# Optimization experiments

Measured on AMD Instinct MI355X. Metric: run time of the kernel, lower is better.

The kernel has to match this reference:

```python
import jax, jax.numpy as jnp
import numpy as np
from jax import lax

B, H, W = 2, 1024, 1024
STRIDE = 32
HF, WF = H // STRIDE, W // STRIDE
C_FM = 2048
A = 9                                       # anchors per location
PRE = 2000                                  # pre-NMS top-k
TOPN = 1000                                 # post-NMS proposals per image
POOL = 7
FC = 256
NUM_CLS = 21
NMS_TH = 0.7


def make_anchors():
    scales = jnp.array([128., 256., 512.])
    ratios = jnp.array([0.5, 1., 2.])
    ws = (scales[:, None] / jnp.sqrt(ratios)[None, :]).reshape(-1)   # [9]
    hs = (scales[:, None] * jnp.sqrt(ratios)[None, :]).reshape(-1)   # [9]
    cx = (jnp.arange(WF) + 0.5) * STRIDE
    cy = (jnp.arange(HF) + 0.5) * STRIDE
    cyg, cxg = jnp.meshgrid(cy, cx, indexing='ij')                   # [HF,WF]
    cxg, cyg = cxg[..., None], cyg[..., None]                        # [HF,WF,1]
    x1 = cxg - ws / 2; y1 = cyg - hs / 2
    x2 = cxg + ws / 2; y2 = cyg + hs / 2
    return jnp.stack([x1, y1, x2, y2], -1).reshape(-1, 4)            # [HF*WF*9,4]


def decode(boxes, deltas):
    w = boxes[..., 2] - boxes[..., 0]
    h = boxes[..., 3] - boxes[..., 1]
    cx = boxes[..., 0] + 0.5 * w
    cy = boxes[..., 1] + 0.5 * h
    dx, dy = deltas[..., 0], deltas[..., 1]
    dw = jnp.clip(deltas[..., 2], -4.0, 4.0)
    dh = jnp.clip(deltas[..., 3], -4.0, 4.0)
    ncx = cx + dx * w; ncy = cy + dy * h
    nw = w * jnp.exp(dw); nh = h * jnp.exp(dh)
    return jnp.stack([ncx - 0.5 * nw, ncy - 0.5 * nh,
                      ncx + 0.5 * nw, ncy + 0.5 * nh], -1)


def clip_boxes(boxes):
    lim = jnp.array([W - 1., H - 1., W - 1., H - 1.])
    return jnp.clip(boxes, 0.0, lim)


def iou_mat(a, b):
    area_a = (a[:, 2] - a[:, 0]) * (a[:, 3] - a[:, 1])
    area_b = (b[:, 2] - b[:, 0]) * (b[:, 3] - b[:, 1])
    lt = jnp.maximum(a[:, None, :2], b[None, :, :2])
    rb = jnp.minimum(a[:, None, 2:], b[None, :, 2:])
    wh = jnp.clip(rb - lt, 0.0)
    inter = wh[..., 0] * wh[..., 1]
    return inter / (area_a[:, None] + area_b[None, :] - inter + 1e-9)


def nms_one(boxes, scores):
    s, idx = lax.top_k(scores, PRE)          # pre-NMS top-k, score-sorted
    b = boxes[idx]                           # [PRE,4]
    iou = iou_mat(b, b)                      # [PRE,PRE]
    ar = jnp.arange(PRE)

    def body(i, keep):
        sup = (iou[i] > NMS_TH) & keep[i] & (ar > i)
        return keep & (~sup)

    keep = lax.fori_loop(0, PRE, body, jnp.ones(PRE, bool))
    ms = jnp.where(keep, s, -1e30)
    s2, j = lax.top_k(ms, TOPN)
    valid = s2 > -1e29
    sel = b[j] * valid[:, None].astype(b.dtype)
    return sel, valid


def roi_align_one(fm, roi):
    # fm: [C,HF,WF], roi: [4] in image coords -> [C,POOL,POOL]
    scale = 1.0 / STRIDE
    x1, y1, x2, y2 = roi[0] * scale, roi[1] * scale, roi[2] * scale, roi[3] * scale
    xs = jnp.clip(x1 + (jnp.arange(POOL) + 0.5) * (x2 - x1) / POOL, 0.0, WF - 1.0)
    ys = jnp.clip(y1 + (jnp.arange(POOL) + 0.5) * (y2 - y1) / POOL, 0.0, HF - 1.0)
    x0 = jnp.floor(xs); y0 = jnp.floor(ys)
    wx = xs - x0; wy = ys - y0
    x0i = x0.astype(jnp.int32); x1i = jnp.minimum(x0i + 1, WF - 1)
    y0i = y0.astype(jnp.int32); y1i = jnp.minimum(y0i + 1, HF - 1)
    gy0 = fm[:, y0i, :]; gy1 = fm[:, y1i, :]          # [C,7,WF]
    f00 = gy0[:, :, x0i]; f01 = gy0[:, :, x1i]        # [C,7,7]
    f10 = gy1[:, :, x0i]; f11 = gy1[:, :, x1i]
    wy_ = wy[None, :, None]; wx_ = wx[None, None, :]
    return (f00 * (1 - wy_) * (1 - wx_) + f01 * (1 - wy_) * wx_
            + f10 * wy_ * (1 - wx_) + f11 * wy_ * wx_)


def conv(x, w, b, stride, padding):
    y = lax.conv_general_dilated(x, w, (stride, stride), padding,
                                 dimension_numbers=('NCHW', 'OIHW', 'NCHW'))
    return y + b[None, :, None, None]


def setup_inputs() -> dict:
    key = jax.random.key(0)
    ks = jax.random.split(key, 12)
    f32 = jnp.float32
    inp = {
        'x': jax.random.normal(ks[0], (B, 3, H, W), f32),
        'backbone_w': jax.random.normal(ks[1], (C_FM, 3, STRIDE, STRIDE), f32) * 0.02,
        'backbone_b': jnp.zeros((C_FM,), f32),
        'rpn_w': jax.random.normal(ks[2], (512, C_FM, 3, 3), f32) * 0.01,
        'rpn_b': jnp.zeros((512,), f32),
        'rpn_cls_w': jax.random.normal(ks[3], (2 * A, 512, 1, 1), f32) * 0.02,
        'rpn_cls_b': jnp.zeros((2 * A,), f32),
        'rpn_reg_w': jax.random.normal(ks[4], (4 * A, 512, 1, 1), f32) * 0.02,
        'rpn_reg_b': jnp.zeros((4 * A,), f32),
        'fc1_w': jax.random.normal(ks[5], (C_FM * POOL * POOL, FC), f32) * 0.005,
        'fc1_b': jnp.zeros((FC,), f32),
        'fc2_w': jax.random.normal(ks[6], (FC, FC), f32) * 0.05,
        'fc2_b': jnp.zeros((FC,), f32),
        'cls_w': jax.random.normal(ks[7], (FC, NUM_CLS), f32) * 0.05,
        'cls_b': jnp.zeros((NUM_CLS,), f32),
        'reg_w': jax.random.normal(ks[8], (FC, 4), f32) * 0.05,
        'reg_b': jnp.zeros((4,), f32),
    }
    return inp


def reference(x, backbone_w, backbone_b, rpn_w, rpn_b, rpn_cls_w, rpn_cls_b,
              rpn_reg_w, rpn_reg_b, fc1_w, fc1_b, fc2_w, fc2_b,
              cls_w, cls_b, reg_w, reg_b):
    # backbone (stride-32 patch conv stand-in for resnet50-small)
    fm = jax.nn.relu(conv(x, backbone_w, backbone_b, STRIDE, 'VALID'))   # [B,2048,32,32]

    anchors = make_anchors()                                             # [N,4], N=HF*WF*9
    anchors = jnp.broadcast_to(anchors, (B,) + anchors.shape)

    # RPN head
    h = jax.nn.relu(conv(fm, rpn_w, rpn_b, 1, 'SAME'))                   # [B,512,32,32]
    cls = conv(h, rpn_cls_w, rpn_cls_b, 1, 'SAME')                       # [B,18,32,32]
    reg = conv(h, rpn_reg_w, rpn_reg_b, 1, 'SAME')                       # [B,36,32,32]
    cls = cls.transpose(0, 2, 3, 1).reshape(B, -1, 2)
    reg = reg.transpose(0, 2, 3, 1).reshape(B, -1, 4)
    fg = jax.nn.softmax(cls, axis=-1)[..., 1]                            # [B,N]

    # proposals: decode -> clip -> NMS filter
    proposals = clip_boxes(decode(anchors, reg))                         # [B,N,4]
    props, valid = jax.vmap(nms_one)(proposals, fg)                      # [B,1000,4], [B,1000]

    # ROI pooling (bilinear, 1 sample/bin, spatial_scale=1/32)
    roi = jax.vmap(jax.vmap(roi_align_one, (None, 0)), (0, 0))(fm, props)  # [B,1000,C,7,7]
    vm = valid.astype(fm.dtype)[..., None]
    roi = roi.reshape(B, TOPN, -1) * vm                                  # [B,1000,100352]

    # detection head
    h1 = jax.nn.relu(jnp.einsum('bnf,fk->bnk', roi, fc1_w) + fc1_b)
    h2 = jax.nn.relu(jnp.einsum('bnk,kj->bnj', h1, fc2_w) + fc2_b)
    cls_scores = (jnp.einsum('bnj,jc->bnc', h2, cls_w) + cls_b) * vm
    reg_preds = (jnp.einsum('bnj,jr->bnr', h2, reg_w) + reg_b) * vm

    detections = clip_boxes(decode(props, reg_preds)) * vm
    return detections, cls_scores
```

## Files before the change

### kernel.cpp

```cpp
#include <hip/hip_runtime.h>

#define PRE 2000
#define TOPN 1000

typedef __attribute__((ext_vector_type(8))) short short8t;
typedef __attribute__((ext_vector_type(4))) float f32x4;
typedef unsigned short ushort_t;

__device__ inline unsigned short bf16_rne(float x) {
    unsigned u = __float_as_uint(x);
    unsigned r = u + 0x7FFFu + ((u >> 16) & 1u);
    return (unsigned short)(r >> 16);
}

__device__ inline void split3_bf16(float x, unsigned short& h, unsigned short& m,
                                   unsigned short& l) {
    h = bf16_rne(x);
    float hf = __uint_as_float((unsigned)h << 16);
    float r1 = x - hf;
    m = bf16_rne(r1);
    float mf = __uint_as_float((unsigned)m << 16);
    l = bf16_rne(r1 - mf);
}


__global__ __launch_bounds__(256, 4) void k_fused(
    const ushort_t* __restrict__ Aq, const ushort_t* __restrict__ Bq,
    ushort_t* __restrict__ T,
    const unsigned* __restrict__ mask, unsigned* __restrict__ keep)
{
    if (blockIdx.x < 2) {
        if (threadIdx.x >= 64) return;
        const int b = blockIdx.x;
        const int lane = threadIdx.x;
        unsigned kw = (lane < 62) ? 0xFFFFFFFFu : (lane == 62 ? 0xFFFFu : 0u);
        const unsigned* mbase = mask + (size_t)b * PRE * 63;
        bool ld = (lane < 63);

        unsigned buf[16];
#pragma unroll
        for (int d = 0; d < 16; d++)
            buf[d] = ld ? mbase[(size_t)d * 63 + lane] : 0u;

        for (int g = 0; g < PRE; g += 16) {
#pragma unroll
            for (int d = 0; d < 16; d++) {
                int i = g + d;
                unsigned row = buf[d];
                int ip = i + 16;
                buf[d] = (ld && ip < PRE) ? mbase[(size_t)ip * 63 + lane] : 0u;
                unsigned wv = (unsigned)__shfl((int)kw, i >> 5);
                if ((wv >> (i & 31)) & 1u)
                    kw &= ~row;
            }
        }
        if (lane < 63) keep[b * 63 + lane] = kw;
        return;
    }

    const int flat = blockIdx.x - 2;
    const int xcd  = flat & 7;
    const int jj   = flat >> 3;
    const int wg   = xcd * 196 + jj;
    const int b    = wg / 784;
    const int rem  = wg - b * 784;
    const int nt   = rem >> 3;
    const int mt   = rem & 7;

    const int tid  = threadIdx.x;
    const int wid  = tid >> 6, lane = tid & 63;
    const int wm_g = (wid >> 1) * 4;
    const int wn_g = (wid & 1) * 4;

    f32x4 acc[4][4];
#pragma unroll
    for (int i = 0; i < 4; i++)
#pragma unroll
        for (int j = 0; j < 4; j++) acc[i][j] = (f32x4){0.f, 0.f, 0.f, 0.f};

    const size_t aoff = (size_t)b * 2097152 + (size_t)mt * 262144
                      + (size_t)wm_g * 512 + (size_t)lane * 8;
    const size_t boff = (size_t)nt * 262144 + (size_t)wn_g * 512 + (size_t)lane * 8;
    const ushort_t* pA = Aq + aoff;
    const ushort_t* pB = Bq + boff;

    for (int ks = 0; ks < 64; ks++) {
        const size_t so = (size_t)ks * 4096;
        short8t a[4], bb[4];
#pragma unroll
        for (int f = 0; f < 4; f++) {
            a[f]  = *(const short8t*)(pA + so + f * 512);
            bb[f] = *(const short8t*)(pB + so + f * 512);
        }
#pragma unroll
        for (int mf = 0; mf < 4; mf++)
#pragma unroll
            for (int nf = 0; nf < 4; nf++)
                acc[mf][nf] = __builtin_amdgcn_mfma_f32_16x16x32_bf16(
                    a[mf], bb[nf], acc[mf][nf], 0, 0, 0);
    }

    ushort_t* Tb = T + (size_t)b * 12845056;
    const int rbase = (lane >> 4) * 4;
    const int lrow  = lane & 15;
#pragma unroll
    for (int mf = 0; mf < 4; mf++) {
#pragma unroll
        for (int nf = 0; nf < 4; nf++) {
            int col = nt * 128 + (wn_g + nf) * 16 + lrow;
#pragma unroll
            for (int r = 0; r < 4; r++) {
                int row = mt * 128 + (wm_g + mf) * 16 + rbase + r;
                Tb[(size_t)row * 12544 + col] = bf16_rne(acc[mf][nf][r]);
            }
        }
    }
}


__global__ __launch_bounds__(256, 2) void k_gemm6(
    const ushort_t* __restrict__ A0, const ushort_t* __restrict__ A1,
    const ushort_t* __restrict__ A2,
    const ushort_t* __restrict__ B0, const ushort_t* __restrict__ B1,
    const ushort_t* __restrict__ B2,
    float* __restrict__ C, int ks_per_z, int KS_TOT, int ldc)
{
    const int tid  = threadIdx.x;
    const int wid  = tid >> 6, lane = tid & 63;
    const int wm_g = (wid >> 1) * 4;
    const int wn_g = (wid & 1) * 4;
    const int mt   = blockIdx.x;
    const int nt   = blockIdx.y;
    const int z    = blockIdx.z;

    f32x4 acc[4][4];
#pragma unroll
    for (int i = 0; i < 4; i++)
#pragma unroll
        for (int j = 0; j < 4; j++) acc[i][j] = (f32x4){0.f, 0.f, 0.f, 0.f};

    const size_t aoff = (size_t)mt * KS_TOT * 4096 + (size_t)wm_g * 512 + (size_t)lane * 8;
    const size_t boff = (size_t)nt * KS_TOT * 4096 + (size_t)wn_g * 512 + (size_t)lane * 8;
    const ushort_t* pA0 = A0 + aoff;
    const ushort_t* pA1 = A1 + aoff;
    const ushort_t* pA2 = A2 + aoff;
    const ushort_t* pB0 = B0 + boff;
    const ushort_t* pB1 = B1 + boff;
    const ushort_t* pB2 = B2 + boff;

    const int ks0 = z * ks_per_z;
    for (int ks = ks0; ks < ks0 + ks_per_z; ks++) {
        const size_t so = (size_t)ks * 4096;
        short8t a0[4], a1[4], a2[4], b0[4], b1[4], b2[4];
#pragma unroll
        for (int f = 0; f < 4; f++) {
            a0[f] = *(const short8t*)(pA0 + so + f * 512);
            a1[f] = *(const short8t*)(pA1 + so + f * 512);
            a2[f] = *(const short8t*)(pA2 + so + f * 512);
            b0[f] = *(const short8t*)(pB0 + so + f * 512);
            b1[f] = *(const short8t*)(pB1 + so + f * 512);
            b2[f] = *(const short8t*)(pB2 + so + f * 512);
        }
#pragma unroll
        for (int mf = 0; mf < 4; mf++)
#pragma unroll
            for (int nf = 0; nf < 4; nf++) {
                f32x4 c = acc[mf][nf];
                c = __builtin_amdgcn_mfma_f32_16x16x32_bf16(a0[mf], b0[nf], c, 0, 0, 0);
                c = __builtin_amdgcn_mfma_f32_16x16x32_bf16(a0[mf], b1[nf], c, 0, 0, 0);
                c = __builtin_amdgcn_mfma_f32_16x16x32_bf16(a1[mf], b0[nf], c, 0, 0, 0);
                c = __builtin_amdgcn_mfma_f32_16x16x32_bf16(a0[mf], b2[nf], c, 0, 0, 0);
                c = __builtin_amdgcn_mfma_f32_16x16x32_bf16(a2[mf], b0[nf], c, 0, 0, 0);
                c = __builtin_amdgcn_mfma_f32_16x16x32_bf16(a1[mf], b1[nf], c, 0, 0, 0);
                acc[mf][nf] = c;
            }
    }

    float* Cz = C + (size_t)z * (gridDim.x * 128) * ldc;
    const int rbase = (lane >> 4) * 4;
    const int lrow  = lane & 15;
#pragma unroll
    for (int mf = 0; mf < 4; mf++) {
#pragma unroll
        for (int nf = 0; nf < 4; nf++) {
            int col = nt * 128 + (wn_g + nf) * 16 + lrow;
#pragma unroll
            for (int r = 0; r < 4; r++) {
                int row = mt * 128 + (wm_g + mf) * 16 + rbase + r;
                Cz[(size_t)row * ldc + col] = acc[mf][nf][r];
            }
        }
    }
}


__global__ void k_convW3(const float* __restrict__ src,
                         ushort_t* __restrict__ D0, ushort_t* __restrict__ D1,
                         ushort_t* __restrict__ D2,
                         int K_LD, int k_base, int KS_TOT)
{
    int t = blockIdx.x * 256 + threadIdx.x;
    int per = KS_TOT << 9;
    int mt = t / per, rem = t - mt * per;
    int ks = rem >> 9, g = (rem >> 6) & 7, l = rem & 63;
    int m  = mt * 128 + g * 16 + (l & 15);
    int k0 = k_base + ks * 32 + ((l >> 4) << 3);
    const float* sp = src + (size_t)m * K_LD + k0;
    short8t v0, v1, v2;
#pragma unroll
    for (int j = 0; j < 8; j++) {
        unsigned short h, mm_, lo;
        split3_bf16(sp[j], h, mm_, lo);
        v0[j] = (short)h; v1[j] = (short)mm_; v2[j] = (short)lo;
    }
    *(short8t*)&D0[(size_t)t * 8] = v0;
    *(short8t*)&D1[(size_t)t * 8] = v1;
    *(short8t*)&D2[(size_t)t * 8] = v2;
}

__global__ void k_convX3(const float* __restrict__ X,
                         ushort_t* __restrict__ D0, ushort_t* __restrict__ D1,
                         ushort_t* __restrict__ D2)
{
    int t = blockIdx.x * 256 + threadIdx.x;
    if (t >= 786432) return;
    int per = 96 << 9;
    int nt = t / per, rem = t - nt * per;
    int ks = rem >> 9, g = (rem >> 6) & 7, l = rem & 63;
    int n  = nt * 128 + g * 16 + (l & 15);
    int bimg = n >> 10, pn = n & 1023;
    int oy = pn >> 5, ox = pn & 31;
    int k0 = ks * 32 + ((l >> 4) << 3);
    int ic = k0 >> 10, kr = k0 & 1023;
    int ky = kr >> 5, kx0 = kr & 31;
    const float* sp = X + (((size_t)(bimg * 3 + ic) * 1024) + oy * 32 + ky) * 1024
                        + ox * 32 + kx0;
    short8t v0, v1, v2;
#pragma unroll
    for (int j = 0; j < 8; j++) {
        unsigned short h, mm_, lo;
        split3_bf16(sp[j], h, mm_, lo);
        v0[j] = (short)h; v1[j] = (short)mm_; v2[j] = (short)lo;
    }
    *(short8t*)&D0[(size_t)t * 8] = v0;
    *(short8t*)&D1[(size_t)t * 8] = v1;
    *(short8t*)&D2[(size_t)t * 8] = v2;
}

__global__ void k_convR3(const float* __restrict__ fm,
                         ushort_t* __restrict__ D0, ushort_t* __restrict__ D1,
                         ushort_t* __restrict__ D2, int k_base, int KS_TOT)
{
    int t = blockIdx.x * 256 + threadIdx.x;
    int per = KS_TOT << 9;
    if (t >= 16 * per) return;
    int nt = t / per, rem = t - nt * per;
    int ks = rem >> 9, g = (rem >> 6) & 7, l = rem & 63;
    int n  = nt * 128 + g * 16 + (l & 15);
    int bimg = n >> 10, pn = n & 1023;
    int y = pn >> 5, x = pn & 31;
    int kg = k_base + ks * 32 + ((l >> 4) << 3);
    int ic = kg / 9;
    int r9 = kg - ic * 9;
    int ky = r9 / 3;
    int kx = r9 - ky * 3;
    short8t v0, v1, v2;
#pragma unroll
    for (int j = 0; j < 8; j++) {
        int yy = y + ky - 1, xx = x + kx - 1;
        float v = 0.f;
        if (yy >= 0 && yy < 32 && xx >= 0 && xx < 32)
            v = fm[(((size_t)(bimg * 2048 + ic)) * 32 + yy) * 32 + xx];
        unsigned short h, mm_, lo;
        split3_bf16(v, h, mm_, lo);
        v0[j] = (short)h; v1[j] = (short)mm_; v2[j] = (short)lo;
        kx++;
        if (kx == 3) { kx = 0; ky++; if (ky == 3) { ky = 0; ic++; } }
    }
    *(short8t*)&D0[(size_t)t * 8] = v0;
    *(short8t*)&D1[(size_t)t * 8] = v1;
    *(short8t*)&D2[(size_t)t * 8] = v2;
}


__global__ void k_convA(const float* __restrict__ fm, ushort_t* __restrict__ Aq)
{
    int t = blockIdx.x * 256 + threadIdx.x;
    if (t >= 524288) return;
    int l  = t & 63;
    int g  = (t >> 6) & 7;
    int ks = (t >> 9) & 63;
    int mt = (t >> 15) & 7;
    int b  = t >> 18;
    int p  = mt * 128 + g * 16 + (l & 15);
    int c0 = ks * 32 + (l >> 4) * 8;
    const float* src = fm + ((size_t)(b * 2048 + c0)) * 1024 + p;
    short8t vh;
#pragma unroll
    for (int j = 0; j < 8; j++) vh[j] = (short)bf16_rne(src[(size_t)j * 1024]);
    *(short8t*)&Aq[(size_t)t * 8] = vh;
}

__global__ void k_convB(const float* __restrict__ W1, ushort_t* __restrict__ Bq)
{
    int t = blockIdx.x * 256 + threadIdx.x;
    if (t >= 3211264) return;
    int l  = t & 63;
    int h_ = (t >> 6) & 7;
    int ks = (t >> 9) & 63;
    int nt = t >> 15;
    int n  = nt * 128 + h_ * 16 + (l & 15);
    int c0 = ks * 32 + (l >> 4) * 8;
    const float* src = W1 + (size_t)c0 * 12544 + n;
    short8t vh;
#pragma unroll
    for (int j = 0; j < 8; j++) vh[j] = (short)bf16_rne(src[(size_t)j * 12544]);
    *(short8t*)&Bq[(size_t)t * 8] = vh;
}


__global__ void k_backbone_reduce(const float* __restrict__ Pb, const float* __restrict__ bias,
                                  float* __restrict__ fm)
{
    int idx = blockIdx.x * 256 + threadIdx.x;
    if (idx >= 2048 * 2048) return;
    int oc = idx >> 11, n = idx & 2047;
    float s = Pb[(size_t)oc * 2048 + n]
            + Pb[((size_t)2048 + oc) * 2048 + n]
            + Pb[((size_t)4096 + oc) * 2048 + n];
    s = fmaxf(s + bias[oc], 0.f);
    int b = n >> 10, p = n & 1023;
    fm[((size_t)b * 2048 + oc) * 1024 + p] = s;
}

__global__ void k_rpn_acc(const float* __restrict__ Cp, float* __restrict__ Racc, int first)
{
    int idx = blockIdx.x * 256 + threadIdx.x;
    if (idx >= 512 * 2048) return;
    float s = 0.f;
#pragma unroll
    for (int z = 0; z < 8; z++)
        s += Cp[(size_t)z * 512 * 2048 + idx];
    Racc[idx] = first ? s : (Racc[idx] + s);
}

__global__ void k_rpn_final(const float* __restrict__ Racc, const float* __restrict__ bias,
                            float* __restrict__ hT)
{
    int idx = blockIdx.x * 256 + threadIdx.x;
    if (idx >= 512 * 2048) return;
    int oc = idx >> 11, n = idx & 2047;
    float s = fmaxf(Racc[(size_t)oc * 2048 + n] + bias[oc], 0.f);
    hT[n * 512 + oc] = s;
}


__global__ __launch_bounds__(64) void k_clsreg(
    const float* __restrict__ hT,
    const float* __restrict__ wc, const float* __restrict__ bc_,
    const float* __restrict__ wr, const float* __restrict__ br_,
    float* __restrict__ cls_raw, float* __restrict__ reg_raw)
{
    __shared__ float s[512];
    int n = blockIdx.x, tid = threadIdx.x;
    const float* hp = hT + n * 512;
    *(float4*)&s[tid * 8]     = *(const float4*)&hp[tid * 8];
    *(float4*)&s[tid * 8 + 4] = *(const float4*)&hp[tid * 8 + 4];
    __syncthreads();
    if (tid < 18) {
        float a = bc_[tid];
        const float* w = wc + tid * 512;
        for (int j = 0; j < 512; j++) a = fmaf(s[j], w[j], a);
        cls_raw[n * 18 + tid] = a;
    } else if (tid < 54) {
        int c = tid - 18;
        float a = br_[c];
        const float* w = wr + c * 512;
        for (int j = 0; j < 512; j++) a = fmaf(s[j], w[j], a);
        reg_raw[n * 36 + c] = a;
    }
}

__global__ void k_proposals(const float* __restrict__ cls_raw, const float* __restrict__ reg_raw,
                            float* __restrict__ proposals, float* __restrict__ scores)
{
    int t = blockIdx.x * 256 + threadIdx.x;
    if (t >= 2 * 9216) return;
    int b = t / 9216, n = t - b * 9216;
    int p = n / 9, a = n - p * 9;
    int pi = b * 1024 + p;
    float c0 = cls_raw[pi * 18 + 2 * a], c1 = cls_raw[pi * 18 + 2 * a + 1];
    float m = fmaxf(c0, c1);
    float e0 = expf(c0 - m), e1 = expf(c1 - m);
    float fg = e1 / (e0 + e1);
    float d0 = reg_raw[pi * 36 + 4 * a + 0];
    float d1 = reg_raw[pi * 36 + 4 * a + 1];
    float d2 = reg_raw[pi * 36 + 4 * a + 2];
    float d3 = reg_raw[pi * 36 + 4 * a + 3];
    int y = p >> 5, x = p & 31;
    const float sc[3] = {128.f, 256.f, 512.f};
    const float rt[3] = {0.5f, 1.f, 2.f};
    int si = a / 3, ri = a - si * 3;
    float sq = sqrtf(rt[ri]);
    float aw = sc[si] / sq, ah = sc[si] * sq;
    float cx = (x + 0.5f) * 32.f, cy = (y + 0.5f) * 32.f;
    float x1 = cx - 0.5f * aw, y1 = cy - 0.5f * ah;
    float x2 = cx + 0.5f * aw, y2 = cy + 0.5f * ah;
    float w = x2 - x1, h = y2 - y1;
    float ccx = x1 + 0.5f * w, ccy = y1 + 0.5f * h;
    float dw = fminf(fmaxf(d2, -4.f), 4.f), dh = fminf(fmaxf(d3, -4.f), 4.f);
    float ncx = ccx + d0 * w, ncy = ccy + d1 * h;
    float nw = w * expf(dw), nh = h * expf(dh);
    float px1 = fminf(fmaxf(ncx - 0.5f * nw, 0.f), 1023.f);
    float py1 = fminf(fmaxf(ncy - 0.5f * nh, 0.f), 1023.f);
    float px2 = fminf(fmaxf(ncx + 0.5f * nw, 0.f), 1023.f);
    float py2 = fminf(fmaxf(ncy + 0.5f * nh, 0.f), 1023.f);
    ((float4*)proposals)[t] = make_float4(px1, py1, px2, py2);
    scores[t] = fg;
}

__global__ void k_sort_init(const float* __restrict__ scores, unsigned long long* __restrict__ keys)
{
    int t = blockIdx.x * 256 + threadIdx.x;
    if (t >= 2 * 16384) return;
    int b = t >> 14, i = t & 16383;
    unsigned long long key = 0ull;
    if (i < 9216) {
        unsigned bits = __float_as_uint(scores[b * 9216 + i]);
        key = ((unsigned long long)bits << 32) | (unsigned)(~i);
    }
    keys[t] = key;
}

__global__ __launch_bounds__(512) void k_sort_lds(unsigned long long* __restrict__ keys,
                                                  int kmode, int wcount)
{
    __shared__ unsigned long long s[4096];
    int b = blockIdx.x / wcount, w = blockIdx.x % wcount;
    unsigned long long* g = keys + b * 16384 + w * 4096;
    int tid = threadIdx.x;
#pragma unroll
    for (int t = 0; t < 8; t++) s[tid + t * 512] = g[tid + t * 512];
    __syncthreads();

    if (kmode == 0) {
        for (unsigned k = 2; k <= 4096; k <<= 1) {
            for (unsigned j = k >> 1; j > 0; j >>= 1) {
#pragma unroll
                for (int t = 0; t < 4; t++) {
                    unsigned p = tid + t * 512;
                    unsigned i = ((p & ~(j - 1)) << 1) | (p & (j - 1));
                    unsigned l = i | j;
                    unsigned gi = (w << 12) + i;
                    bool up = ((gi & k) == 0);
                    unsigned long long a = s[i], c = s[l];
                    bool sw = up ? (c > a) : (a > c);
                    if (sw) { s[i] = c; s[l] = a; }
                }
                __syncthreads();
            }
        }
    } else {
        unsigned k = (unsigned)kmode;
        for (unsigned j = 2048; j > 0; j >>= 1) {
#pragma unroll
            for (int t = 0; t < 4; t++) {
                unsigned p = tid + t * 512;
                unsigned i = ((p & ~(j - 1)) << 1) | (p & (j - 1));
                unsigned l = i | j;
                unsigned gi = (w << 12) + i;
                bool up = ((gi & k) == 0);
                unsigned long long a = s[i], c = s[l];
                bool sw = up ? (c > a) : (a > c);
                if (sw) { s[i] = c; s[l] = a; }
            }
            __syncthreads();
        }
    }
#pragma unroll
    for (int t = 0; t < 8; t++) g[tid + t * 512] = s[tid + t * 512];
}

__global__ void k_sort_global(unsigned long long* __restrict__ keys, int kk, int jj)
{
    int t = blockIdx.x * 256 + threadIdx.x;
    if (t >= 2 * 8192) return;
    int b = t >> 13;
    unsigned p = t & 8191;
    unsigned j = (unsigned)jj, k = (unsigned)kk;
    unsigned i = ((p & ~(j - 1)) << 1) | (p & (j - 1));
    unsigned l = i | j;
    bool up = ((i & k) == 0);
    unsigned long long* g = keys + b * 16384;
    unsigned long long a = g[i], c = g[l];
    bool sw = up ? (c > a) : (a > c);
    if (sw) { g[i] = c; g[l] = a; }
}

__global__ void k_gather_top(const unsigned long long* __restrict__ keys,
                             const float* __restrict__ proposals, float* __restrict__ topBoxes)
{
    int t = blockIdx.x * 256 + threadIdx.x;
    if (t >= 2 * PRE) return;
    int b = t / PRE, pos = t - b * PRE;
    unsigned long long key = keys[b * 16384 + pos];
    unsigned idx = ~(unsigned)(key & 0xFFFFFFFFull);
    ((float4*)topBoxes)[t] = ((const float4*)proposals)[b * 9216 + idx];
}

__global__ __launch_bounds__(64) void k_iou(const float* __restrict__ topBoxes,
                                            unsigned* __restrict__ mask)
{
    int blk = blockIdx.x;
    int b = blk / PRE, i = blk - b * PRE;
    int lane = threadIdx.x;
    const float4* boxes = ((const float4*)topBoxes) + b * PRE;
    float4 bi = boxes[i];
    float area_a = (bi.z - bi.x) * (bi.w - bi.y);
    if (lane < 63) {
        unsigned wbits = 0u;
        for (int t = 0; t < 32; t++) {
            int j = lane * 32 + t;
            if (j < PRE && j > i) {
                float4 bj = boxes[j];
                float area_b = (bj.z - bj.x) * (bj.w - bj.y);
                float ltx = fmaxf(bi.x, bj.x), lty = fmaxf(bi.y, bj.y);
                float rbx = fminf(bi.z, bj.z), rby = fminf(bi.w, bj.w);
                float iw = fmaxf(rbx - ltx, 0.f), ih = fmaxf(rby - lty, 0.f);
                float inter = iw * ih;
                float iou = inter / (area_a + area_b - inter + 1e-9f);
                if (iou > 0.7f) wbits |= (1u << t);
            }
        }
        mask[(b * PRE + i) * 63 + lane] = wbits;
    }
}

__global__ __launch_bounds__(64) void k_compact(const unsigned* __restrict__ keep,
                                                const float* __restrict__ topBoxes,
                                                float* __restrict__ props, float* __restrict__ validf)
{
    int b = blockIdx.x;
    int lane = threadIdx.x;
    unsigned kw = (lane < 63) ? keep[b * 63 + lane] : 0u;
    int cnt = __popc(kw);
    int inc = cnt;
    for (int off = 1; off < 64; off <<= 1) {
        int v = __shfl_up(inc, off);
        if (lane >= off) inc += v;
    }
    int excl = inc - cnt;
    for (int t = 0; t < 32; t++) {
        if ((kw >> t) & 1u) {
            int rank = excl + __popc(kw & ((1u << t) - 1u));
            if (rank < TOPN) {
                int j = lane * 32 + t;
                ((float4*)props)[b * TOPN + rank] = ((const float4*)topBoxes)[b * PRE + j];
                validf[b * TOPN + rank] = 1.0f;
            }
        }
    }
}

__global__ void k_roico(const float* __restrict__ props, const float* __restrict__ validf,
                        float* __restrict__ roico)
{
    int t = blockIdx.x * 256 + threadIdx.x;
    if (t >= 2 * TOPN) return;
    float* rc = roico + t * 48;
    if (validf[t] == 0.f) {
        for (int u = 0; u < 48; u++) rc[u] = 0.f;
        return;
    }
    float4 box = ((const float4*)props)[t];
    const float scale = 1.f / 32.f;
    float x1 = box.x * scale, y1 = box.y * scale, x2 = box.z * scale, y2 = box.w * scale;
    for (int u = 0; u < 7; u++) {
        float xs = x1 + (u + 0.5f) * (x2 - x1) / 7.f;
        xs = fminf(fmaxf(xs, 0.f), 31.f);
        float x0f = floorf(xs);
        rc[u] = x0f;
        rc[7 + u] = fminf(x0f + 1.f, 31.f);
        rc[14 + u] = xs - x0f;
        float ys = y1 + (u + 0.5f) * (y2 - y1) / 7.f;
        ys = fminf(fmaxf(ys, 0.f), 31.f);
        float y0f = floorf(ys);
        rc[21 + u] = y0f;
        rc[28 + u] = fminf(y0f + 1.f, 31.f);
        rc[35 + u] = ys - y0f;
    }
}

__global__ __launch_bounds__(256) void k_combine(
    const ushort_t* __restrict__ T, const float* __restrict__ roico,
    const float* __restrict__ validf, const float* __restrict__ b1,
    float* __restrict__ h1)
{
    int g = blockIdx.x;
    int b = g / TOPN;
    int tid = threadIdx.x;
    __shared__ float rc[48];
    if (tid < 48) rc[tid] = roico[(size_t)g * 48 + tid];
    __syncthreads();
    float acc = 0.f;
    float vm = validf[g];
    const ushort_t* Tb = T + (size_t)b * 12845056;
    if (vm != 0.f) {
#pragma unroll
        for (int py = 0; py < 7; py++) {
            int y0 = (int)rc[21 + py], y1 = (int)rc[28 + py];
            float wy = rc[35 + py];
#pragma unroll
            for (int px = 0; px < 7; px++) {
                int x0 = (int)rc[px], x1 = (int)rc[7 + px];
                float wx = rc[14 + px];
                int qo = (py * 7 + px) * 256 + tid;
                float f00 = __uint_as_float((unsigned)Tb[(size_t)(y0 * 32 + x0) * 12544 + qo] << 16);
                float f01 = __uint_as_float((unsigned)Tb[(size_t)(y0 * 32 + x1) * 12544 + qo] << 16);
                float f10 = __uint_as_float((unsigned)Tb[(size_t)(y1 * 32 + x0) * 12544 + qo] << 16);
                float f11 = __uint_as_float((unsigned)Tb[(size_t)(y1 * 32 + x1) * 12544 + qo] << 16);
                acc += f00 * (1.f - wy) * (1.f - wx) + f01 * (1.f - wy) * wx
                     + f10 * wy * (1.f - wx) + f11 * wy * wx;
            }
        }
    }
    h1[(size_t)g * 256 + tid] = fmaxf(acc + b1[tid], 0.f);
}

__global__ __launch_bounds__(256) void k_head(
    const float* __restrict__ h1,
    const float* __restrict__ w2, const float* __restrict__ b2,
    const float* __restrict__ wc, const float* __restrict__ bcb,
    const float* __restrict__ wr, const float* __restrict__ brb,
    const float* __restrict__ props, const float* __restrict__ validf,
    float* __restrict__ out)
{
    int g = blockIdx.x;
    int tid = threadIdx.x;
    __shared__ float s1[256], s2v[256], rg[4];
    s1[tid] = h1[(size_t)g * 256 + tid];
    __syncthreads();
    float acc = b2[tid];
    for (int j = 0; j < 256; j++) acc = fmaf(s1[j], w2[j * 256 + tid], acc);
    s2v[tid] = fmaxf(acc, 0.f);
    __syncthreads();
    float vm = validf[g];
    if (tid < 21) {
        float a = bcb[tid];
        for (int j = 0; j < 256; j++) a = fmaf(s2v[j], wc[j * 21 + tid], a);
        out[8000 + g * 21 + tid] = a * vm;
    } else if (tid >= 32 && tid < 36) {
        int r = tid - 32;
        float a = brb[r];
        for (int j = 0; j < 256; j++) a = fmaf(s2v[j], wr[j * 4 + r], a);
        rg[r] = a * vm;
    }
    __syncthreads();
    if (tid == 0) {
        float4 pb = ((const float4*)props)[g];
        float w = pb.z - pb.x, h = pb.w - pb.y;
        float cx = pb.x + 0.5f * w, cy = pb.y + 0.5f * h;
        float dw = fminf(fmaxf(rg[2], -4.f), 4.f), dh = fminf(fmaxf(rg[3], -4.f), 4.f);
        float ncx = cx + rg[0] * w, ncy = cy + rg[1] * h;
        float nw = w * expf(dw), nh = h * expf(dh);
        float x1 = fminf(fmaxf(ncx - 0.5f * nw, 0.f), 1023.f);
        float y1 = fminf(fmaxf(ncy - 0.5f * nh, 0.f), 1023.f);
        float x2 = fminf(fmaxf(ncx + 0.5f * nw, 0.f), 1023.f);
        float y2 = fminf(fmaxf(ncy + 0.5f * nh, 0.f), 1023.f);
        ((float4*)out)[g] = make_float4(x1 * vm, y1 * vm, x2 * vm, y2 * vm);
    }
}


extern "C" void kernel_launch(void* const* d_in, const int* in_sizes, int n_in,
                              void* d_out, int out_size, void* d_ws, size_t ws_size,
                              hipStream_t stream)
{
    const float* x          = (const float*)d_in[0];
    const float* backbone_w = (const float*)d_in[1];
    const float* backbone_b = (const float*)d_in[2];
    const float* rpn_w      = (const float*)d_in[3];
    const float* rpn_b      = (const float*)d_in[4];
    const float* rpn_cls_w  = (const float*)d_in[5];
    const float* rpn_cls_b  = (const float*)d_in[6];
    const float* rpn_reg_w  = (const float*)d_in[7];
    const float* rpn_reg_b  = (const float*)d_in[8];
    const float* fc1_w      = (const float*)d_in[9];
    const float* fc1_b      = (const float*)d_in[10];
    const float* fc2_w      = (const float*)d_in[11];
    const float* fc2_b      = (const float*)d_in[12];
    const float* cls_w      = (const float*)d_in[13];
    const float* cls_b      = (const float*)d_in[14];
    const float* reg_w      = (const float*)d_in[15];
    const float* reg_b      = (const float*)d_in[16];
    float* out = (float*)d_out;

    char* base = (char*)d_ws;
    size_t off = 0;
    auto alloc = [&](size_t bytes) {
        void* p = base + off;
        off = (off + bytes + 255) & ~(size_t)255;
        return p;
    };
    float* fm        = (float*)alloc((size_t)2 * 2048 * 1024 * 4);
    float* Cp        = (float*)alloc((size_t)16 * 512 * 2048 * 4);
    float* hT        = (float*)alloc(2048u * 512 * 4);
    float* Racc      = (float*)alloc(512u * 2048 * 4);
    float* cls_raw   = (float*)alloc(2048u * 18 * 4);
    float* reg_raw   = (float*)alloc(2048u * 36 * 4);
    float* proposals = (float*)alloc(2u * 9216 * 4 * 4);
    float* scores    = (float*)alloc(2u * 9216 * 4);
    unsigned long long* keys = (unsigned long long*)alloc(2u * 16384 * 8);
    float* topBoxes  = (float*)alloc(2u * PRE * 4 * 4);
    unsigned* ioumask= (unsigned*)alloc(2u * PRE * 63 * 4);
    unsigned* keep   = (unsigned*)alloc(2u * 63 * 4);
    float* props     = (float*)alloc(2u * TOPN * 4 * 4);
    float* validf    = (float*)alloc(2u * TOPN * 4);
    float* roico     = (float*)alloc(2u * TOPN * 48 * 4);
    char*  arena     = (char*)alloc(119537664);
    float* h1        = (float*)alloc(2u * TOPN * 256 * 4);

    ushort_t* Wb0 = (ushort_t*)(arena);
    ushort_t* Wb1 = (ushort_t*)(arena + 12582912);
    ushort_t* Wb2 = (ushort_t*)(arena + 25165824);
    ushort_t* Xf0 = (ushort_t*)(arena + 37748736);
    ushort_t* Xf1 = (ushort_t*)(arena + 50331648);
    ushort_t* Xf2 = (ushort_t*)(arena + 62914560);
    ushort_t* Wr0 = (ushort_t*)(arena);
    ushort_t* Wr1 = (ushort_t*)(arena + 4718592);
    ushort_t* Wr2 = (ushort_t*)(arena + 9437184);
    ushort_t* Rb0 = (ushort_t*)(arena + 14155776);
    ushort_t* Rb1 = (ushort_t*)(arena + 33030144);
    ushort_t* Rb2 = (ushort_t*)(arena + 51904512);
    ushort_t* Aq   = (ushort_t*)(arena);
    ushort_t* Tbuf = (ushort_t*)(arena + 16777216);
    ushort_t* Bq   = (ushort_t*)Cp;

    k_convW3<<<3072, 256, 0, stream>>>(backbone_w, Wb0, Wb1, Wb2, 3072, 0, 96);
    k_convX3<<<3072, 256, 0, stream>>>(x, Xf0, Xf1, Xf2);
    k_gemm6<<<dim3(16, 16, 3), 256, 0, stream>>>(Wb0, Wb1, Wb2, Xf0, Xf1, Xf2,
                                                 Cp, 32, 96, 2048);
    k_backbone_reduce<<<(2048 * 2048) / 256, 256, 0, stream>>>(Cp, backbone_b, fm);

    for (int q = 0; q < 4; q++) {
        k_convW3<<<1152, 256, 0, stream>>>(rpn_w, Wr0, Wr1, Wr2, 18432, q * 4608, 144);
        k_convR3<<<4608, 256, 0, stream>>>(fm, Rb0, Rb1, Rb2, q * 4608, 144);
        k_gemm6<<<dim3(4, 16, 8), 256, 0, stream>>>(Wr0, Wr1, Wr2, Rb0, Rb1, Rb2,
                                                    Cp, 18, 144, 2048);
        k_rpn_acc<<<4096, 256, 0, stream>>>(Cp, Racc, q == 0 ? 1 : 0);
    }
    k_rpn_final<<<4096, 256, 0, stream>>>(Racc, rpn_b, hT);

    k_convB<<<12544, 256, 0, stream>>>(fc1_w, Bq);
    k_convA<<<2048, 256, 0, stream>>>(fm, Aq);

    k_clsreg<<<2048, 64, 0, stream>>>(hT, rpn_cls_w, rpn_cls_b, rpn_reg_w, rpn_reg_b,
                                      cls_raw, reg_raw);
    k_proposals<<<(2 * 9216 + 255) / 256, 256, 0, stream>>>(cls_raw, reg_raw, proposals, scores);

    k_sort_init<<<(2 * 16384) / 256, 256, 0, stream>>>(scores, keys);
    k_sort_lds<<<8, 512, 0, stream>>>(keys, 0, 4);
    k_sort_global<<<64, 256, 0, stream>>>(keys, 8192, 4096);
    k_sort_lds<<<8, 512, 0, stream>>>(keys, 8192, 4);
    k_sort_global<<<64, 256, 0, stream>>>(keys, 16384, 8192);
    k_sort_global<<<64, 256, 0, stream>>>(keys, 16384, 4096);
    k_sort_lds<<<2, 512, 0, stream>>>(keys, 16384, 1);
    k_gather_top<<<(2 * PRE + 255) / 256, 256, 0, stream>>>(keys, proposals, topBoxes);

    k_iou<<<2 * PRE, 64, 0, stream>>>(topBoxes, ioumask);
    hipMemsetAsync(props, 0, 2u * TOPN * 4 * 4, stream);
    hipMemsetAsync(validf, 0, 2u * TOPN * 4, stream);

    k_fused<<<1570, 256, 0, stream>>>(Aq, Bq, Tbuf, ioumask, keep);

    k_compact<<<2, 64, 0, stream>>>(keep, topBoxes, props, validf);
    k_roico<<<(2 * TOPN + 255) / 256, 256, 0, stream>>>(props, validf, roico);
    k_combine<<<2 * TOPN, 256, 0, stream>>>(Tbuf, roico, validf, fc1_b, h1);
    k_head<<<2 * TOPN, 256, 0, stream>>>(h1, fc2_w, fc2_b, cls_w, cls_b, reg_w, reg_b,
                                         props, validf, out);
}
```

Baseline: 922.5 us.

## Merge full-bitonic top-k sort into one kernel and fuse ROI-coord, FC1 and head

The multi-kernel bitonic sort (key init, LDS passes, global merge passes and top-2000 gather) becomes one kernel per image. It builds keys, sorts all 16384 entries in 128 KB of dynamic shared memory and gathers the top boxes directly. The ROI coordinate computation, the FC1 combine and the detection head are fused into a single per-ROI kernel, so the roico and h1 buffers no longer go through global memory. This removes many small launches and intermediate traffic, but the sort now runs on only two workgroups and relies on a large dynamic LDS allocation.

Measured after the change: 979.3 us. +6.2%, slower.

```diff
diff --git a/kernel.cpp b/kernel.cpp
--- a/kernel.cpp
+++ b/kernel.cpp
@@ -419,57 +419,33 @@
     scores[t] = fg;
 }
 
-__global__ void k_sort_init(const float* __restrict__ scores, unsigned long long* __restrict__ keys)
-{
-    int t = blockIdx.x * 256 + threadIdx.x;
-    if (t >= 2 * 16384) return;
-    int b = t >> 14, i = t & 16383;
-    unsigned long long key = 0ull;
-    if (i < 9216) {
-        unsigned bits = __float_as_uint(scores[b * 9216 + i]);
-        key = ((unsigned long long)bits << 32) | (unsigned)(~i);
-    }
-    keys[t] = key;
-}
-
-__global__ __launch_bounds__(512) void k_sort_lds(unsigned long long* __restrict__ keys,
-                                                  int kmode, int wcount)
-{
-    __shared__ unsigned long long s[4096];
-    int b = blockIdx.x / wcount, w = blockIdx.x % wcount;
-    unsigned long long* g = keys + b * 16384 + w * 4096;
-    int tid = threadIdx.x;
-#pragma unroll
-    for (int t = 0; t < 8; t++) s[tid + t * 512] = g[tid + t * 512];
+
+__global__ __launch_bounds__(1024) void k_sortfull(
+    const float* __restrict__ scores, const float* __restrict__ proposals,
+    float* __restrict__ topBoxes)
+{
+    extern __shared__ unsigned long long s[];
+    const int b = blockIdx.x;
+    const int tid = threadIdx.x;
+
+    for (int i = tid; i < 16384; i += 1024) {
+        unsigned long long key = 0ull;
+        if (i < 9216) {
+            unsigned bits = __float_as_uint(scores[b * 9216 + i]);
+            key = ((unsigned long long)bits << 32) | (unsigned)(~i);
+        }
+        s[i] = key;
+    }
     __syncthreads();
 
-    if (kmode == 0) {
-        for (unsigned k = 2; k <= 4096; k <<= 1) {
-            for (unsigned j = k >> 1; j > 0; j >>= 1) {
-#pragma unroll
-                for (int t = 0; t < 4; t++) {
-                    unsigned p = tid + t * 512;
-                    unsigned i = ((p & ~(j - 1)) << 1) | (p & (j - 1));
-                    unsigned l = i | j;
-                    unsigned gi = (w << 12) + i;
-                    bool up = ((gi & k) == 0);
-                    unsigned long long a = s[i], c = s[l];
-                    bool sw = up ? (c > a) : (a > c);
-                    if (sw) { s[i] = c; s[l] = a; }
-                }
-                __syncthreads();
-            }
-        }
-    } else {
-        unsigned k = (unsigned)kmode;
-        for (unsigned j = 2048; j > 0; j >>= 1) {
-#pragma unroll
-            for (int t = 0; t < 4; t++) {
-                unsigned p = tid + t * 512;
+    for (unsigned k = 2; k <= 16384; k <<= 1) {
+        for (unsigned j = k >> 1; j > 0; j >>= 1) {
+#pragma unroll
+            for (int t = 0; t < 8; t++) {
+                unsigned p = tid + t * 1024;
                 unsigned i = ((p & ~(j - 1)) << 1) | (p & (j - 1));
                 unsigned l = i | j;
-                unsigned gi = (w << 12) + i;
-                bool up = ((gi & k) == 0);
+                bool up = ((i & k) == 0);
                 unsigned long long a = s[i], c = s[l];
                 bool sw = up ? (c > a) : (a > c);
                 if (sw) { s[i] = c; s[l] = a; }
@@ -477,35 +453,12 @@
             __syncthreads();
         }
     }
-#pragma unroll
-    for (int t = 0; t < 8; t++) g[tid + t * 512] = s[tid + t * 512];
-}
-
-__global__ void k_sort_global(unsigned long long* __restrict__ keys, int kk, int jj)
-{
-    int t = blockIdx.x * 256 + threadIdx.x;
-    if (t >= 2 * 8192) return;
-    int b = t >> 13;
-    unsigned p = t & 8191;
-    unsigned j = (unsigned)jj, k = (unsigned)kk;
-    unsigned i = ((p & ~(j - 1)) << 1) | (p & (j - 1));
-    unsigned l = i | j;
-    bool up = ((i & k) == 0);
-    unsigned long long* g = keys + b * 16384;
-    unsigned long long a = g[i], c = g[l];
-    bool sw = up ? (c > a) : (a > c);
-    if (sw) { g[i] = c; g[l] = a; }
-}
-
-__global__ void k_gather_top(const unsigned long long* __restrict__ keys,
-                             const float* __restrict__ proposals, float* __restrict__ topBoxes)
-{
-    int t = blockIdx.x * 256 + threadIdx.x;
-    if (t >= 2 * PRE) return;
-    int b = t / PRE, pos = t - b * PRE;
-    unsigned long long key = keys[b * 16384 + pos];
-    unsigned idx = ~(unsigned)(key & 0xFFFFFFFFull);
-    ((float4*)topBoxes)[t] = ((const float4*)proposals)[b * 9216 + idx];
+
+    for (int pos = tid; pos < PRE; pos += 1024) {
+        unsigned long long key = s[pos];
+        unsigned idx = ~(unsigned)(key & 0xFFFFFFFFull);
+        ((float4*)topBoxes)[b * PRE + pos] = ((const float4*)proposals)[b * 9216 + idx];
+    }
 }
 
 __global__ __launch_bounds__(64) void k_iou(const float* __restrict__ topBoxes,
@@ -562,48 +515,48 @@
     }
 }
 
-__global__ void k_roico(const float* __restrict__ props, const float* __restrict__ validf,
-                        float* __restrict__ roico)
-{
-    int t = blockIdx.x * 256 + threadIdx.x;
-    if (t >= 2 * TOPN) return;
-    float* rc = roico + t * 48;
-    if (validf[t] == 0.f) {
-        for (int u = 0; u < 48; u++) rc[u] = 0.f;
-        return;
-    }
-    float4 box = ((const float4*)props)[t];
-    const float scale = 1.f / 32.f;
-    float x1 = box.x * scale, y1 = box.y * scale, x2 = box.z * scale, y2 = box.w * scale;
-    for (int u = 0; u < 7; u++) {
-        float xs = x1 + (u + 0.5f) * (x2 - x1) / 7.f;
-        xs = fminf(fmaxf(xs, 0.f), 31.f);
-        float x0f = floorf(xs);
-        rc[u] = x0f;
-        rc[7 + u] = fminf(x0f + 1.f, 31.f);
-        rc[14 + u] = xs - x0f;
-        float ys = y1 + (u + 0.5f) * (y2 - y1) / 7.f;
-        ys = fminf(fmaxf(ys, 0.f), 31.f);
-        float y0f = floorf(ys);
-        rc[21 + u] = y0f;
-        rc[28 + u] = fminf(y0f + 1.f, 31.f);
-        rc[35 + u] = ys - y0f;
-    }
-}
-
-__global__ __launch_bounds__(256) void k_combine(
-    const ushort_t* __restrict__ T, const float* __restrict__ roico,
+
+__global__ __launch_bounds__(256) void k_combhead(
+    const ushort_t* __restrict__ T, const float* __restrict__ props,
     const float* __restrict__ validf, const float* __restrict__ b1,
-    float* __restrict__ h1)
+    const float* __restrict__ w2, const float* __restrict__ b2,
+    const float* __restrict__ wc, const float* __restrict__ bcb,
+    const float* __restrict__ wr, const float* __restrict__ brb,
+    float* __restrict__ out)
 {
     int g = blockIdx.x;
     int b = g / TOPN;
     int tid = threadIdx.x;
     __shared__ float rc[48];
-    if (tid < 48) rc[tid] = roico[(size_t)g * 48 + tid];
+    __shared__ float s1[256], s2v[256], rg[4];
+
+    float vm = validf[g];
+    if (vm != 0.f && tid < 14) {
+        float4 box = ((const float4*)props)[g];
+        const float scale = 1.f / 32.f;
+        float x1 = box.x * scale, y1 = box.y * scale;
+        float x2 = box.z * scale, y2 = box.w * scale;
+        if (tid < 7) {
+            int u = tid;
+            float xs = x1 + (u + 0.5f) * (x2 - x1) / 7.f;
+            xs = fminf(fmaxf(xs, 0.f), 31.f);
+            float x0f = floorf(xs);
+            rc[u] = x0f;
+            rc[7 + u] = fminf(x0f + 1.f, 31.f);
+            rc[14 + u] = xs - x0f;
+        } else {
+            int u = tid - 7;
+            float ys = y1 + (u + 0.5f) * (y2 - y1) / 7.f;
+            ys = fminf(fmaxf(ys, 0.f), 31.f);
+            float y0f = floorf(ys);
+            rc[21 + u] = y0f;
+            rc[28 + u] = fminf(y0f + 1.f, 31.f);
+            rc[35 + u] = ys - y0f;
+        }
+    }
     __syncthreads();
+
     float acc = 0.f;
-    float vm = validf[g];
     const ushort_t* Tb = T + (size_t)b * 12845056;
     if (vm != 0.f) {
 #pragma unroll
@@ -624,27 +577,13 @@
             }
         }
     }
-    h1[(size_t)g * 256 + tid] = fmaxf(acc + b1[tid], 0.f);
-}
-
-__global__ __launch_bounds__(256) void k_head(
-    const float* __restrict__ h1,
-    const float* __restrict__ w2, const float* __restrict__ b2,
-    const float* __restrict__ wc, const float* __restrict__ bcb,
-    const float* __restrict__ wr, const float* __restrict__ brb,
-    const float* __restrict__ props, const float* __restrict__ validf,
-    float* __restrict__ out)
-{
-    int g = blockIdx.x;
-    int tid = threadIdx.x;
-    __shared__ float s1[256], s2v[256], rg[4];
-    s1[tid] = h1[(size_t)g * 256 + tid];
+    s1[tid] = fmaxf(acc + b1[tid], 0.f);
     __syncthreads();
-    float acc = b2[tid];
-    for (int j = 0; j < 256; j++) acc = fmaf(s1[j], w2[j * 256 + tid], acc);
-    s2v[tid] = fmaxf(acc, 0.f);
+
+    float a2 = b2[tid];
+    for (int j = 0; j < 256; j++) a2 = fmaf(s1[j], w2[j * 256 + tid], a2);
+    s2v[tid] = fmaxf(a2, 0.f);
     __syncthreads();
-    float vm = validf[g];
     if (tid < 21) {
         float a = bcb[tid];
         for (int j = 0; j < 256; j++) a = fmaf(s2v[j], wc[j * 21 + tid], a);
@@ -719,6 +658,7 @@
     float* roico     = (float*)alloc(2u * TOPN * 48 * 4);
     char*  arena     = (char*)alloc(119537664);
     float* h1        = (float*)alloc(2u * TOPN * 256 * 4);
+    (void)keys; (void)roico; (void)h1;
 
     ushort_t* Wb0 = (ushort_t*)(arena);
     ushort_t* Wb1 = (ushort_t*)(arena + 12582912);
@@ -758,14 +698,7 @@
                                       cls_raw, reg_raw);
     k_proposals<<<(2 * 9216 + 255) / 256, 256, 0, stream>>>(cls_raw, reg_raw, proposals, scores);
 
-    k_sort_init<<<(2 * 16384) / 256, 256, 0, stream>>>(scores, keys);
-    k_sort_lds<<<8, 512, 0, stream>>>(keys, 0, 4);
-    k_sort_global<<<64, 256, 0, stream>>>(keys, 8192, 4096);
-    k_sort_lds<<<8, 512, 0, stream>>>(keys, 8192, 4);
-    k_sort_global<<<64, 256, 0, stream>>>(keys, 16384, 8192);
-    k_sort_global<<<64, 256, 0, stream>>>(keys, 16384, 4096);
-    k_sort_lds<<<2, 512, 0, stream>>>(keys, 16384, 1);
-    k_gather_top<<<(2 * PRE + 255) / 256, 256, 0, stream>>>(keys, proposals, topBoxes);
+    k_sortfull<<<2, 1024, 131072, stream>>>(scores, proposals, topBoxes);
 
     k_iou<<<2 * PRE, 64, 0, stream>>>(topBoxes, ioumask);
     hipMemsetAsync(props, 0, 2u * TOPN * 4 * 4, stream);
@@ -774,8 +707,7 @@
     k_fused<<<1570, 256, 0, stream>>>(Aq, Bq, Tbuf, ioumask, keep);
 
     k_compact<<<2, 64, 0, stream>>>(keep, topBoxes, props, validf);
-    k_roico<<<(2 * TOPN + 255) / 256, 256, 0, stream>>>(props, validf, roico);
-    k_combine<<<2 * TOPN, 256, 0, stream>>>(Tbuf, roico, validf, fc1_b, h1);
-    k_head<<<2 * TOPN, 256, 0, stream>>>(h1, fc2_w, fc2_b, cls_w, cls_b, reg_w, reg_b,
-                                         props, validf, out);
-}
+    k_combhead<<<2 * TOPN, 256, 0, stream>>>(Tbuf, props, validf, fc1_b,
+                                             fc2_w, fc2_b, cls_w, cls_b, reg_w, reg_b,
+                                             out);
+}
```
